# Optimization experiments

Hardware: AMD Instinct MI355X
Metric: run time of the kernel (lower is better)

## Reference

```python
import jax, jax.numpy as jnp
import numpy as np

D, K, N_NODES, E_DIM, H, L, HEADS, FF = 1024, 128, 200000, 384, 128, 2, 4, 128


def setup_inputs() -> dict:
    key = jax.random.key(0)
    ks = jax.random.split(key, 12)
    # regular graph: target node 0 has D neighbors (nodes 1..D); each neighbor n
    # has exactly K incoming edges, the first from tgt, the rest from random src != 0
    src = jax.random.randint(ks[0], (D, K), 1, N_NODES, dtype=jnp.int32)
    src = src.at[:, 0].set(0)
    dst = jnp.broadcast_to(jnp.arange(1, D + 1, dtype=jnp.int32)[:, None], (D, K))
    edge_index = jnp.stack([src.reshape(-1), dst.reshape(-1)])
    s = 0.05
    return {
        "tgt_x_index": jnp.zeros((1,), jnp.int32),
        "x": jax.random.normal(ks[1], (N_NODES, 64), jnp.float32),
        "edge_index": edge_index,
        "edge_attrs": jax.random.normal(ks[2], (D * K, E_DIM), jnp.float32),
        "first_token_marker": jax.random.normal(ks[3], (H,), jnp.float32),
        "proj_w": jax.random.normal(ks[4], (H, E_DIM), jnp.float32) * s,
        "proj_b": jnp.zeros((H,), jnp.float32),
        "attn_in_w": jax.random.normal(ks[5], (L, 3 * H, H), jnp.float32) * s,
        "attn_in_b": jnp.zeros((L, 3 * H), jnp.float32),
        "attn_out_w": jax.random.normal(ks[6], (L, H, H), jnp.float32) * s,
        "attn_out_b": jnp.zeros((L, H), jnp.float32),
        "ln1_g": jnp.ones((L, H), jnp.float32),
        "ln1_b": jnp.zeros((L, H), jnp.float32),
        "ff1_w": jax.random.normal(ks[7], (L, FF, H), jnp.float32) * s,
        "ff1_b": jnp.zeros((L, FF), jnp.float32),
        "ff2_w": jax.random.normal(ks[8], (L, H, FF), jnp.float32) * s,
        "ff2_b": jnp.zeros((L, H), jnp.float32),
        "ln2_g": jnp.ones((L, H), jnp.float32),
        "ln2_b": jnp.zeros((L, H), jnp.float32),
        "pred_w1": jax.random.normal(ks[9], (H, H), jnp.float32) * s,
        "pred_b1": jnp.zeros((H,), jnp.float32),
        "pred_w2": jax.random.normal(ks[10], (1, H), jnp.float32) * s,
        "pred_b2": jnp.zeros((1,), jnp.float32),
        "num_neighbors": D,
        "seq_len": K,
    }


def _ln(x, g, b):
    m = x.mean(-1, keepdims=True)
    v = ((x - m) ** 2).mean(-1, keepdims=True)
    return (x - m) * jax.lax.rsqrt(v + 1e-5) * g + b


def _forward(tgt_x_index, x, edge_index, edge_attrs, first_token_marker,
             proj_w, proj_b, attn_in_w, attn_in_b, attn_out_w, attn_out_b,
             ln1_g, ln1_b, ff1_w, ff1_b, ff2_w, ff2_b, ln2_g, ln2_b,
             pred_w1, pred_b1, pred_w2, pred_b2, num_neighbors, seq_len):
    tgt = tgt_x_index[0]
    src, dst = edge_index[0], edge_index[1]
    is_tgt = src == tgt
    # neighbors of target, in edge order (torch: edge_index[1][edge_index[0]==tgt])
    neigh_idx = jnp.nonzero(is_tgt, size=num_neighbors)[0]
    neigh_nodes = dst[neigh_idx]                       # [D]
    # fused ragged gather: map each edge to its neighbor slot, sort so that each
    # neighbor's edges are contiguous with the tgt->n edge first (stable sort
    # preserves original edge order within groups, matching boolean-mask gather)
    slot = jnp.full((x.shape[0],), num_neighbors, jnp.int32).at[neigh_nodes].set(
        jnp.arange(num_neighbors, dtype=jnp.int32))
    eslot = slot[dst]                                  # [E]
    sort_key = eslot.astype(jnp.int64) * 2 + jnp.where(is_tgt, 0, 1)
    order = jnp.argsort(sort_key)[: num_neighbors * seq_len]
    rows = edge_attrs[order].reshape(num_neighbors, seq_len, edge_attrs.shape[-1])
    hidden = proj_w.shape[0]
    hd = hidden // HEADS
    h = rows @ proj_w.T + proj_b                       # [D, K, H]
    h = h.at[:, 0, :].add(first_token_marker)          # first-token marker
    n_layers = attn_in_w.shape[0]
    for l in range(n_layers):
        qkv = h @ attn_in_w[l].T + attn_in_b[l]        # [D, K, 3H]
        q, k_, v = jnp.split(qkv, 3, axis=-1)
        q = q.reshape(num_neighbors, seq_len, HEADS, hd)
        k_ = k_.reshape(num_neighbors, seq_len, HEADS, hd)
        v = v.reshape(num_neighbors, seq_len, HEADS, hd)
        att = jax.nn.softmax(
            jnp.einsum('bqhd,bkhd->bhqk', q, k_) / jnp.sqrt(jnp.float32(hd)), axis=-1)
        o = jnp.einsum('bhqk,bkhd->bqhd', att, v).reshape(num_neighbors, seq_len, hidden)
        h = _ln(h + o @ attn_out_w[l].T + attn_out_b[l], ln1_g[l], ln1_b[l])
        f = jax.nn.relu(h @ ff1_w[l].T + ff1_b[l]) @ ff2_w[l].T + ff2_b[l]
        h = _ln(h + f, ln2_g[l], ln2_b[l])
    pooled = h.mean(axis=1)                            # mean over seq -> [D, H]
    final = pooled.mean(axis=0, keepdims=True)         # mean over neighbors -> [1, H]
    hmid = jax.nn.relu(final @ pred_w1.T + pred_b1)
    return jax.nn.sigmoid(hmid @ pred_w2.T + pred_b2)  # [1, 1]


def reference(tgt_x_index, x, edge_index, edge_attrs, first_token_marker,
              proj_w, proj_b, attn_in_w, attn_in_b, attn_out_w, attn_out_b,
              ln1_g, ln1_b, ff1_w, ff1_b, ff2_w, ff2_b, ln2_g, ln2_b,
              pred_w1, pred_b1, pred_w2, pred_b2, num_neighbors, seq_len):
    return _forward(tgt_x_index, x, edge_index, edge_attrs, first_token_marker,
                    proj_w, proj_b, attn_in_w, attn_in_b, attn_out_w, attn_out_b,
                    ln1_g, ln1_b, ff1_w, ff1_b, ff2_w, ff2_b, ln2_g, ln2_b,
                    pred_w1, pred_b1, pred_w2, pred_b2, num_neighbors, seq_len)
```

## Files before the change

### kernel.cpp

```cpp
#include <hip/hip_runtime.h>
#include <cstdint>
#include <cstddef>

#define D_N     1024
#define K_S     128
#define EDIM    384
#define HID     128
#define NHEAD   4
#define HDIM    32
#define FFD     128
#define NLAYER  2
#define ETOT    (D_N * K_S)
#define NNODES  200000
#define NBINS   (2 * D_N + 2)
#define NCH     512
#define CHL     (ETOT / NCH)

#define OFF_ORDER 0u
#define OFF_KEY   (1u << 19)
#define OFF_SLOT  (1u << 20)
#define OFF_HIST  (1u << 21)
#define OFF_TOT   (OFF_HIST + NBINS * NCH * 4)
#define OFF_POOL  (7u << 20)
#define OFF_WBF   OFF_HIST
#define WP_OFF 0
#define WI_OFF 49152
#define WO_OFF 147456
#define W1_OFF 180224
#define W2_OFF 212992
#define WTOT   245760

typedef __attribute__((ext_vector_type(8))) short  bf16x8;
typedef __attribute__((ext_vector_type(4))) short  short4v;
typedef __attribute__((ext_vector_type(4))) float  f32x4;

__device__ __forceinline__ short f2bf(float f) {
    union { float f; unsigned u; } v; v.f = f;
    unsigned r = v.u + 0x7fffu + ((v.u >> 16) & 1u);
    return (short)(r >> 16);
}
__device__ __forceinline__ int swz_off(int r, int byteInRow, int strideBytes) {
    return (r * strideBytes + byteInRow) ^ ((r & 7) << 4);
}

__global__ void init_ws(int* __restrict__ slot, int* __restrict__ hist)
{
    int idx = blockIdx.x * blockDim.x + threadIdx.x;
    int stride = gridDim.x * blockDim.x;
    for (int i = idx; i < NBINS * NCH; i += stride) hist[i] = 0;
    for (int i = idx; i < NNODES; i += stride) slot[i] = D_N;
}

__global__ void find_neigh(const int* __restrict__ eidx,
                           const int* __restrict__ tgt_idx,
                           int* __restrict__ slot)
{
    __shared__ int wtot[16];
    __shared__ int wbase_s[16];
    __shared__ int neigh[D_N];
    const int tid  = threadIdx.x;
    const int lane = tid & 63;
    const int wv   = tid >> 6;
    const int tgt  = tgt_idx[0];
    const int* src = eidx;
    const int* dst = eidx + ETOT;
    const int epc  = ETOT / 1024;
    const int e0   = tid * epc;

    int c = 0;
    const int4* s4 = (const int4*)(src + e0);
    #pragma unroll 8
    for (int i = 0; i < epc / 4; ++i) {
        int4 v = s4[i];
        c += (v.x == tgt) + (v.y == tgt) + (v.z == tgt) + (v.w == tgt);
    }
    int incl = c;
    #pragma unroll
    for (int d = 1; d < 64; d <<= 1) {
        int t = __shfl_up(incl, d, 64);
        if (lane >= d) incl += t;
    }
    if (lane == 63) wtot[wv] = incl;
    __syncthreads();
    if (tid < 16) {
        int s = 0;
        for (int j = 0; j < tid; ++j) s += wtot[j];
        wbase_s[tid] = s;
    }
    __syncthreads();
    int r = wbase_s[wv] + incl - c;
    for (int e = e0; e < e0 + epc; ++e) {
        if (src[e] == tgt) { if (r < D_N) neigh[r] = dst[e]; ++r; }
    }
    __syncthreads();
    int total = wbase_s[15] + wtot[15];
    if (tid < total && tid < D_N) slot[neigh[tid]] = tid;
}

__global__ void compute_key(const int* __restrict__ eidx,
                            const int* __restrict__ tgt_idx,
                            const int* __restrict__ slot,
                            int* __restrict__ key)
{
    int e = blockIdx.x * 256 + threadIdx.x;
    if (e >= ETOT) return;
    int tgt = tgt_idx[0];
    key[e] = slot[eidx[ETOT + e]] * 2 + ((eidx[e] != tgt) ? 1 : 0);
}

__global__ void hist_build(const int* __restrict__ key, int* __restrict__ hist)
{
    const int c = blockIdx.x * 256 + threadIdx.x;
    if (c >= NCH) return;
    const int4* kp = (const int4*)(key + c * CHL);
    int cur = -1, run = 0;
    for (int i = 0; i < CHL / 4; ++i) {
        int4 k4 = kp[i];
        #pragma unroll
        for (int j = 0; j < 4; ++j) {
            int k = (j == 0) ? k4.x : (j == 1) ? k4.y : (j == 2) ? k4.z : k4.w;
            if (k == cur) { ++run; }
            else {
                if (run) hist[cur * NCH + c] += run;
                cur = k; run = 1;
            }
        }
    }
    if (run) hist[cur * NCH + c] += run;
}

__global__ void scan_pass1(const int* __restrict__ hist, int* __restrict__ tot)
{
    int b = blockIdx.x * 256 + threadIdx.x;
    if (b >= NBINS) return;
    const int4* h = (const int4*)(hist + b * NCH);
    int s = 0;
    #pragma unroll 4
    for (int c = 0; c < NCH / 4; ++c) { int4 v = h[c]; s += v.x + v.y + v.z + v.w; }
    tot[b] = s;
}

#define SCN 2176
__global__ void scan_pass2(int* __restrict__ tot)
{
    __shared__ int A[SCN];
    __shared__ int B[SCN];
    const int tid = threadIdx.x;
    for (int i = tid; i < SCN; i += 1024) A[i] = (i < NBINS) ? tot[i] : 0;
    __syncthreads();
    int* cur = A; int* nxt = B;
    for (int s = 1; s < SCN; s <<= 1) {
        for (int i = tid; i < SCN; i += 1024) nxt[i] = (i >= s) ? cur[i] + cur[i - s] : cur[i];
        __syncthreads();
        int* t = cur; cur = nxt; nxt = t;
    }
    for (int i = tid; i < NBINS; i += 1024) tot[i] = (i == 0) ? 0 : cur[i - 1];
}

__global__ void scan_pass3(int* __restrict__ hist, const int* __restrict__ base)
{
    const int wvg  = (blockIdx.x * blockDim.x + threadIdx.x) >> 6;
    const int lane = threadIdx.x & 63;
    if (wvg >= NBINS) return;
    int* h = hist + wvg * NCH + lane * 8;
    int4 a = *(int4*)h;
    int4 b4 = *(int4*)(h + 4);
    int ls = a.x + a.y + a.z + a.w + b4.x + b4.y + b4.z + b4.w;
    int incl = ls;
    #pragma unroll
    for (int d = 1; d < 64; d <<= 1) {
        int t = __shfl_up(incl, d, 64);
        if (lane >= d) incl += t;
    }
    int run = base[wvg] + incl - ls;
    int4 o1, o2;
    o1.x = run; run += a.x;  o1.y = run; run += a.y;
    o1.z = run; run += a.z;  o1.w = run; run += a.w;
    o2.x = run; run += b4.x; o2.y = run; run += b4.y;
    o2.z = run; run += b4.z; o2.w = run; run += b4.w;
    *(int4*)h = o1;
    *(int4*)(h + 4) = o2;
}

__global__ void scatter_order(const int* __restrict__ key,
                              int* __restrict__ hist,
                              int* __restrict__ order)
{
    const int c = blockIdx.x * 256 + threadIdx.x;
    if (c >= NCH) return;
    const int e0 = c * CHL;
    const int4* kp = (const int4*)(key + e0);
    int cur = -1, pos = 0;
    for (int i = 0; i < CHL / 4; ++i) {
        int4 k4 = kp[i];
        #pragma unroll
        for (int j = 0; j < 4; ++j) {
            int k = (j == 0) ? k4.x : (j == 1) ? k4.y : (j == 2) ? k4.z : k4.w;
            if (k != cur) {
                if (cur >= 0) hist[cur * NCH + c] = pos;
                cur = k;
                pos = hist[k * NCH + c];
            }
            if (pos >= 0 && pos < ETOT) order[pos] = e0 + i * 4 + j;
            ++pos;
        }
    }
    if (cur >= 0) hist[cur * NCH + c] = pos;
}

__global__ void cvt_all(const float* __restrict__ p0, const float* __restrict__ p1,
                        const float* __restrict__ p2, const float* __restrict__ p3,
                        const float* __restrict__ p4, short* __restrict__ wbf)
{
    int i = (blockIdx.x * 256 + threadIdx.x) * 8;
    if (i >= WTOT) return;
    const float* s;
    if      (i < WI_OFF) s = p0 + i;
    else if (i < WO_OFF) s = p1 + (i - WI_OFF);
    else if (i < W1_OFF) s = p2 + (i - WO_OFF);
    else if (i < W2_OFF) s = p3 + (i - W1_OFF);
    else                 s = p4 + (i - W2_OFF);
    float4 a = *(const float4*)s;
    float4 b = *(const float4*)(s + 4);
    bf16x8 o;
    o[0] = f2bf(a.x); o[1] = f2bf(a.y); o[2] = f2bf(a.z); o[3] = f2bf(a.w);
    o[4] = f2bf(b.x); o[5] = f2bf(b.y); o[6] = f2bf(b.z); o[7] = f2bf(b.w);
    *(bf16x8*)(wbf + i) = o;
}

template<int CF, int KC, typename GetB>
__device__ __forceinline__ void gemm1(f32x4 (&acc)[CF],
    const char* aB, int aRow0, int aStride, int l15, int g, GetB getB)
{
    #pragma unroll
    for (int kc = 0; kc < KC; ++kc) {
        bf16x8 a = *(const bf16x8*)(aB + swz_off(aRow0 + l15, kc * 64 + g * 16, aStride));
        #pragma unroll
        for (int cf = 0; cf < CF; ++cf)
            acc[cf] = __builtin_amdgcn_mfma_f32_16x16x32_bf16(a, getB(cf, kc), acc[cf], 0, 0, 0);
    }
}

template<int ROWB>
__device__ __forceinline__ void stage_w(const char* __restrict__ gsrc, char* ldst,
                                        int nbytes, int tid)
{
    #pragma unroll 4
    for (int u = tid * 16; u < nbytes; u += 512 * 16) {
        int row = u / ROWB;
        int in  = u - row * ROWB;
        *(bf16x8*)(ldst + swz_off(row, in, ROWB)) = *(const bf16x8*)(gsrc + u);
    }
}

__device__ __forceinline__ void layer_norm1(f32x4 (&x)[8],
    const float* __restrict__ gg, const float* __restrict__ bb, int l15)
{
    float gv[8], bv[8];
    #pragma unroll
    for (int cf = 0; cf < 8; ++cf) { gv[cf] = gg[l15 + 16 * cf]; bv[cf] = bb[l15 + 16 * cf]; }
    #pragma unroll
    for (int rg = 0; rg < 4; ++rg) {
        float s = 0.f;
        #pragma unroll
        for (int cf = 0; cf < 8; ++cf) s += x[cf][rg];
        s += __shfl_xor(s, 1); s += __shfl_xor(s, 2);
        s += __shfl_xor(s, 4); s += __shfl_xor(s, 8);
        float mean = s * (1.f / 128.f);
        float v = 0.f;
        #pragma unroll
        for (int cf = 0; cf < 8; ++cf) { float d = x[cf][rg] - mean; v += d * d; }
        v += __shfl_xor(v, 1); v += __shfl_xor(v, 2);
        v += __shfl_xor(v, 4); v += __shfl_xor(v, 8);
        float rs = rsqrtf(v * (1.f / 128.f) + 1e-5f);
        #pragma unroll
        for (int cf = 0; cf < 8; ++cf)
            x[cf][rg] = (x[cf][rg] - mean) * rs * gv[cf] + bv[cf];
    }
}

#define LDS_TOTAL 163840
__global__ __launch_bounds__(512, 2) void fused_mfma(
    const float* __restrict__ edge_attrs,
    const float* __restrict__ ftm,
    const short* __restrict__ wP, const float* __restrict__ projb,
    const short* __restrict__ wI, const float* __restrict__ aib,
    const short* __restrict__ wO, const float* __restrict__ aob,
    const float* __restrict__ l1g, const float* __restrict__ l1b,
    const short* __restrict__ w1, const float* __restrict__ f1b,
    const short* __restrict__ w2, const float* __restrict__ f2b,
    const float* __restrict__ l2g, const float* __restrict__ l2b,
    const int*   __restrict__ order,
    float*       __restrict__ pooled)
{
    __shared__ __align__(16) char sm[LDS_TOTAL];
    char* hbf  = sm;
    char* wbuf = sm + 32768;
    char* act  = sm + 131072;
    char* k_l  = act;
    char* vT   = act + 8192;
    char* qOh  = act + 16384;
    char* Pch  = act + 24576;
    char* ebuf = act;
    char* ffb  = act;
    float* pool_s = (float*)act;

    const int tid  = threadIdx.x;
    const int w    = tid >> 6;
    const int l    = tid & 63;
    const int l15  = l & 15;
    const int g    = l >> 4;
    const int row0 = 16 * w;
    const int b    = blockIdx.x;

    f32x4 hx[8];

    {
        #pragma unroll
        for (int cf = 0; cf < 8; ++cf) {
            float bs = projb[l15 + 16 * cf];
            hx[cf] = (f32x4){bs, bs, bs, bs};
        }
        const int r_off = l >> 2;
        const int coff  = (l & 3) * 32;
        const int row   = row0 + r_off;
        const int rowIdx = order[b * K_S + row];
        const float* arow = edge_attrs + (size_t)rowIdx * EDIM;

        float4 v[8];
        #pragma unroll
        for (int j = 0; j < 8; ++j) v[j] = *(const float4*)(arow + coff + j * 4);

        stage_w<768>((const char*)wP, wbuf, 98304, tid);
        __syncthreads();

        #pragma unroll
        for (int ch = 0; ch < 3; ++ch) {
            #pragma unroll
            for (int j = 0; j < 4; ++j) {
                float4 a = v[2 * j], c = v[2 * j + 1];
                bf16x8 pk;
                pk[0] = f2bf(a.x); pk[1] = f2bf(a.y); pk[2] = f2bf(a.z); pk[3] = f2bf(a.w);
                pk[4] = f2bf(c.x); pk[5] = f2bf(c.y); pk[6] = f2bf(c.z); pk[7] = f2bf(c.w);
                *(bf16x8*)(ebuf + swz_off(row, coff * 2 + j * 16, 256)) = pk;
            }
            if (ch < 2) {
                #pragma unroll
                for (int j = 0; j < 8; ++j)
                    v[j] = *(const float4*)(arow + (ch + 1) * 128 + coff + j * 4);
            }
            gemm1<8, 4>(hx, ebuf, row0, 256, l15, g,
                [&](int cf, int kc) {
                    return *(const bf16x8*)(wbuf +
                        swz_off(l15 + 16 * cf, ch * 256 + kc * 64 + g * 16, 768));
                });
        }
        if (w == 0 && g == 0) {
            #pragma unroll
            for (int cf = 0; cf < 8; ++cf) hx[cf][0] += ftm[l15 + 16 * cf];
        }
        #pragma unroll
        for (int cf = 0; cf < 8; ++cf)
            #pragma unroll
            for (int rg = 0; rg < 4; ++rg)
                *(short*)(hbf + swz_off(row0 + g * 4 + rg, (l15 + 16 * cf) * 2, 256)) =
                    f2bf(hx[cf][rg]);
    }
    __syncthreads();

    for (int ly = 0; ly < NLAYER; ++ly) {
        const short* WIl = wI + (size_t)ly * 3 * HID * HID;
        const float* bI  = aib + ly * 3 * HID;
        const short* WOl = wO + (size_t)ly * HID * HID;
        const float* bO  = aob + ly * HID;
        const short* W1l = w1 + (size_t)ly * FFD * HID;
        const float* b1  = f1b + ly * FFD;
        const short* W2l = w2 + (size_t)ly * HID * FFD;
        const float* b2v = f2b + ly * HID;

        stage_w<256>((const char*)WIl, wbuf, 98304, tid);

        #pragma unroll
        for (int cf = 0; cf < 8; ++cf) {
            float bs = bO[l15 + 16 * cf];
            #pragma unroll
            for (int rg = 0; rg < 4; ++rg) hx[cf][rg] += bs;
        }
        __syncthreads();

        for (int hd = 0; hd < NHEAD; ++hd) {
            f32x4 acc[6];
            #pragma unroll
            for (int cf = 0; cf < 6; ++cf) {
                float bs = bI[(cf >> 1) * HID + hd * HDIM + l15 + 16 * (cf & 1)];
                acc[cf] = (f32x4){bs, bs, bs, bs};
            }
            gemm1<6, 4>(acc, hbf, row0, 256, l15, g,
                [&](int cf, int kc) {
                    int colw = (cf >> 1) * HID + hd * HDIM + l15 + 16 * (cf & 1);
                    return *(const bf16x8*)(wbuf + swz_off(colw, kc * 64 + g * 16, 256));
                });
            #pragma unroll
            for (int cf = 0; cf < 2; ++cf) {
                int dcol = (l15 + 16 * cf) * 2;
                #pragma unroll
                for (int rg = 0; rg < 4; ++rg) {
                    int row = row0 + g * 4 + rg;
                    *(short*)(qOh + swz_off(row, dcol, 64)) = f2bf(acc[cf][rg]);
                    *(short*)(k_l + swz_off(row, dcol, 64)) = f2bf(acc[2 + cf][rg]);
                }
                short4v pv;
                pv[0] = f2bf(acc[4 + cf][0]); pv[1] = f2bf(acc[4 + cf][1]);
                pv[2] = f2bf(acc[4 + cf][2]); pv[3] = f2bf(acc[4 + cf][3]);
                *(short4v*)(vT + swz_off(l15 + 16 * cf, (row0 + g * 4) * 2, 256)) = pv;
            }
            __syncthreads();

            f32x4 sc[8];
            #pragma unroll
            for (int cf = 0; cf < 8; ++cf) sc[cf] = (f32x4){0.f, 0.f, 0.f, 0.f};
            gemm1<8, 1>(sc, qOh, row0, 64, l15, g,
                [&](int cf, int kc) {
                    (void)kc;
                    return *(const bf16x8*)(k_l + swz_off(l15 + 16 * cf, g * 16, 64));
                });

            const float SC_ = 0.17677669529663687f;
            float inv_s[4];
            #pragma unroll
            for (int rg = 0; rg < 4; ++rg) {
                float mx = -1e30f;
                #pragma unroll
                for (int cf = 0; cf < 8; ++cf) {
                    sc[cf][rg] *= SC_;
                    mx = fmaxf(mx, sc[cf][rg]);
                }
                mx = fmaxf(mx, __shfl_xor(mx, 1)); mx = fmaxf(mx, __shfl_xor(mx, 2));
                mx = fmaxf(mx, __shfl_xor(mx, 4)); mx = fmaxf(mx, __shfl_xor(mx, 8));
                float sum = 0.f;
                #pragma unroll
                for (int cf = 0; cf < 8; ++cf) {
                    float e = __expf(sc[cf][rg] - mx);
                    sc[cf][rg] = e; sum += e;
                }
                sum += __shfl_xor(sum, 1); sum += __shfl_xor(sum, 2);
                sum += __shfl_xor(sum, 4); sum += __shfl_xor(sum, 8);
                inv_s[rg] = 1.f / sum;
            }

            f32x4 ov[2];
            ov[0] = (f32x4){0.f, 0.f, 0.f, 0.f};
            ov[1] = (f32x4){0.f, 0.f, 0.f, 0.f};
            #pragma unroll
            for (int cc = 0; cc < 4; ++cc) {
                #pragma unroll
                for (int q = 0; q < 2; ++q) {
                    int cfi = 2 * cc + q;
                    #pragma unroll
                    for (int rg = 0; rg < 4; ++rg)
                        *(short*)(Pch + swz_off(row0 + g * 4 + rg, (l15 + 16 * q) * 2, 64)) =
                            f2bf(sc[cfi][rg] * inv_s[rg]);
                }
                gemm1<2, 1>(ov, Pch, row0, 64, l15, g,
                    [&](int cf, int kc) {
                        (void)kc;
                        return *(const bf16x8*)(vT + swz_off(l15 + 16 * cf, cc * 64 + g * 16, 256));
                    });
            }
            #pragma unroll
            for (int cf = 0; cf < 2; ++cf)
                #pragma unroll
                for (int rg = 0; rg < 4; ++rg)
                    *(short*)(qOh + swz_off(row0 + g * 4 + rg, (l15 + 16 * cf) * 2, 64)) =
                        f2bf(ov[cf][rg]);
            gemm1<8, 1>(hx, qOh, row0, 64, l15, g,
                [&](int cf, int kc) {
                    (void)kc;
                    int col = l15 + 16 * cf;
                    return *(const bf16x8*)(WOl + (size_t)col * HID + hd * HDIM + g * 8);
                });
            __syncthreads();
        }

        stage_w<256>((const char*)W1l, wbuf,         32768, tid);
        stage_w<256>((const char*)W2l, wbuf + 32768, 32768, tid);

        layer_norm1(hx, l1g + ly * HID, l1b + ly * HID, l15);
        #pragma unroll
        for (int cf = 0; cf < 8; ++cf)
            #pragma unroll
            for (int rg = 0; rg < 4; ++rg)
                *(short*)(hbf + swz_off(row0 + g * 4 + rg, (l15 + 16 * cf) * 2, 256)) =
                    f2bf(hx[cf][rg]);
        __syncthreads();

        f32x4 ff[8];
        #pragma unroll
        for (int cf = 0; cf < 8; ++cf) {
            float bs = b1[l15 + 16 * cf];
            ff[cf] = (f32x4){bs, bs, bs, bs};
        }
        gemm1<8, 4>(ff, hbf, row0, 256, l15, g,
            [&](int cf, int kc) {
                return *(const bf16x8*)(wbuf + swz_off(l15 + 16 * cf, kc * 64 + g * 16, 256));
            });
        #pragma unroll
        for (int cf = 0; cf < 8; ++cf)
            #pragma unroll
            for (int rg = 0; rg < 4; ++rg)
                *(short*)(ffb + swz_off(row0 + g * 4 + rg, (l15 + 16 * cf) * 2, 256)) =
                    f2bf(fmaxf(ff[cf][rg], 0.f));

        f32x4 yy[8];
        #pragma unroll
        for (int cf = 0; cf < 8; ++cf) {
            float bs = b2v[l15 + 16 * cf];
            yy[cf] = (f32x4){bs, bs, bs, bs};
        }
        gemm1<8, 4>(yy, ffb, row0, 256, l15, g,
            [&](int cf, int kc) {
                return *(const bf16x8*)(wbuf + 32768 +
                    swz_off(l15 + 16 * cf, kc * 64 + g * 16, 256));
            });
        #pragma unroll
        for (int cf = 0; cf < 8; ++cf) yy[cf] += hx[cf];
        layer_norm1(yy, l2g + ly * HID, l2b + ly * HID, l15);
        #pragma unroll
        for (int cf = 0; cf < 8; ++cf) {
            hx[cf] = yy[cf];
            #pragma unroll
            for (int rg = 0; rg < 4; ++rg)
                *(short*)(hbf + swz_off(row0 + g * 4 + rg, (l15 + 16 * cf) * 2, 256)) =
                    f2bf(yy[cf][rg]);
        }
        __syncthreads();
    }

    #pragma unroll
    for (int cf = 0; cf < 8; ++cf) {
        float s = hx[cf][0] + hx[cf][1] + hx[cf][2] + hx[cf][3];
        s += __shfl_xor(s, 16); s += __shfl_xor(s, 32);
        if (g == 0) pool_s[w * 128 + l15 + 16 * cf] = s;
    }
    __syncthreads();
    if (tid < 128) {
        float s = 0.f;
        #pragma unroll
        for (int ww = 0; ww < 8; ++ww) s += pool_s[ww * 128 + tid];
        pooled[b * HID + tid] = s * (1.f / 128.f);
    }
}

__global__ void final_pred(const float* __restrict__ pooled,
                           const float* __restrict__ w1, const float* __restrict__ b1,
                           const float* __restrict__ w2, const float* __restrict__ b2,
                           float* __restrict__ out)
{
    __shared__ float part[4][HID];
    __shared__ float fin[HID];
    __shared__ float hm[HID];
    const int tid = threadIdx.x;
    const int f = tid & 127, q = tid >> 7;
    float s = 0.f;
    for (int bb = q * 256; bb < (q + 1) * 256; ++bb) s += pooled[bb * HID + f];
    part[q][f] = s;
    __syncthreads();
    if (tid < HID) {
        fin[tid] = (part[0][tid] + part[1][tid] + part[2][tid] + part[3][tid])
                   * (1.f / (float)D_N);
    }
    __syncthreads();
    if (tid < HID) {
        float a = b1[tid];
        for (int k = 0; k < HID; ++k) a += fin[k] * w1[tid * HID + k];
        hm[tid] = fmaxf(a, 0.f) * w2[tid];
    }
    __syncthreads();
    if (tid == 0) {
        float z = 0.f;
        for (int j = 0; j < HID; ++j) z += hm[j];
        z += b2[0];
        out[0] = 1.f / (1.f + __expf(-z));
    }
}

extern "C" void kernel_launch(void* const* d_in, const int* in_sizes, int n_in,
                              void* d_out, int out_size, void* d_ws, size_t ws_size,
                              hipStream_t stream)
{
    (void)in_sizes; (void)n_in; (void)out_size; (void)ws_size;

    const int*   tgt   = (const int*)  d_in[0];
    const int*   eidx  = (const int*)  d_in[2];
    const float* eattr = (const float*)d_in[3];
    const float* ftm   = (const float*)d_in[4];
    const float* projw = (const float*)d_in[5];
    const float* projb = (const float*)d_in[6];
    const float* aiw   = (const float*)d_in[7];
    const float* aib   = (const float*)d_in[8];
    const float* aow   = (const float*)d_in[9];
    const float* aob   = (const float*)d_in[10];
    const float* l1g   = (const float*)d_in[11];
    const float* l1b   = (const float*)d_in[12];
    const float* f1w   = (const float*)d_in[13];
    const float* f1b   = (const float*)d_in[14];
    const float* f2w   = (const float*)d_in[15];
    const float* f2b   = (const float*)d_in[16];
    const float* l2g   = (const float*)d_in[17];
    const float* l2b   = (const float*)d_in[18];
    const float* pw1   = (const float*)d_in[19];
    const float* pb1   = (const float*)d_in[20];
    const float* pw2   = (const float*)d_in[21];
    const float* pb2   = (const float*)d_in[22];

    char* ws = (char*)d_ws;
    int*   order  = (int*)  (ws + OFF_ORDER);
    int*   key    = (int*)  (ws + OFF_KEY);
    int*   slot   = (int*)  (ws + OFF_SLOT);
    int*   hist   = (int*)  (ws + OFF_HIST);
    int*   tot    = (int*)  (ws + OFF_TOT);
    float* pooled = (float*)(ws + OFF_POOL);
    short* wbf    = (short*)(ws + OFF_WBF);

    init_ws      <<<dim3(1024), dim3(256),  0, stream>>>(slot, hist);
    find_neigh   <<<dim3(1),    dim3(1024), 0, stream>>>(eidx, tgt, slot);
    compute_key  <<<dim3(512),  dim3(256),  0, stream>>>(eidx, tgt, slot, key);
    hist_build   <<<dim3(2),    dim3(256),  0, stream>>>(key, hist);
    scan_pass1   <<<dim3(9),    dim3(256),  0, stream>>>(hist, tot);
    scan_pass2   <<<dim3(1),    dim3(1024), 0, stream>>>(tot);
    scan_pass3   <<<dim3(513),  dim3(256),  0, stream>>>(hist, tot);
    scatter_order<<<dim3(2),    dim3(256),  0, stream>>>(key, hist, order);
    cvt_all      <<<dim3(120),  dim3(256),  0, stream>>>(projw, aiw, aow, f1w, f2w, wbf);

    fused_mfma<<<dim3(D_N), dim3(512), 0, stream>>>(
        eattr, ftm,
        wbf + WP_OFF, projb,
        wbf + WI_OFF, aib,
        wbf + WO_OFF, aob,
        l1g, l1b,
        wbf + W1_OFF, f1b,
        wbf + W2_OFF, f2b,
        l2g, l2b,
        order, pooled);

    final_pred<<<dim3(1), dim3(512), 0, stream>>>(pooled, pw1, pb1, pw2, pb2, (float*)d_out);
}
```

Before: 521.2 us.

## Read bf16 weights directly from global, shrink LDS, fuse init and convert kernels

Stops staging the projection, attention and FFN weights into LDS and has the MFMA B operands load straight from global/L2 memory. This cuts LDS from 160KB to 80KB, which lets more blocks fit per CU. Heads are now processed in pairs with one barrier per pair, and the weight conversion is merged into the workspace-init kernel, removing one launch. The risk is more global and L2 traffic with uncoalesced B-fragment loads in every GEMM. The workspace offsets are rearranged so the weight buffer no longer overlaps the histogram.

```diff
diff --git a/kernel.cpp b/kernel.cpp
--- a/kernel.cpp
+++ b/kernel.cpp
@@ -17,12 +17,12 @@
 #define CHL     (ETOT / NCH)
 
 #define OFF_ORDER 0u
-#define OFF_KEY   (1u << 19)
-#define OFF_SLOT  (1u << 20)
-#define OFF_HIST  (1u << 21)
-#define OFF_TOT   (OFF_HIST + NBINS * NCH * 4)
-#define OFF_POOL  (7u << 20)
-#define OFF_WBF   OFF_HIST
+#define OFF_KEY   0x080000u
+#define OFF_SLOT  0x100000u
+#define OFF_HIST  0x200000u
+#define OFF_TOT   0x601800u
+#define OFF_WBF   0x604000u
+#define OFF_POOL  0x680000u
 #define WP_OFF 0
 #define WI_OFF 49152
 #define WO_OFF 147456
@@ -43,12 +43,30 @@
     return (r * strideBytes + byteInRow) ^ ((r & 7) << 4);
 }
 
-__global__ void init_ws(int* __restrict__ slot, int* __restrict__ hist)
+__global__ void init_cvt(int* __restrict__ slot, int* __restrict__ hist,
+                         const float* __restrict__ p0, const float* __restrict__ p1,
+                         const float* __restrict__ p2, const float* __restrict__ p3,
+                         const float* __restrict__ p4, short* __restrict__ wbf)
 {
     int idx = blockIdx.x * blockDim.x + threadIdx.x;
     int stride = gridDim.x * blockDim.x;
     for (int i = idx; i < NBINS * NCH; i += stride) hist[i] = 0;
     for (int i = idx; i < NNODES; i += stride) slot[i] = D_N;
+    int i = idx * 8;
+    if (i < WTOT) {
+        const float* s;
+        if      (i < WI_OFF) s = p0 + i;
+        else if (i < WO_OFF) s = p1 + (i - WI_OFF);
+        else if (i < W1_OFF) s = p2 + (i - WO_OFF);
+        else if (i < W2_OFF) s = p3 + (i - W1_OFF);
+        else                 s = p4 + (i - W2_OFF);
+        float4 a = *(const float4*)s;
+        float4 b = *(const float4*)(s + 4);
+        bf16x8 o;
+        o[0] = f2bf(a.x); o[1] = f2bf(a.y); o[2] = f2bf(a.z); o[3] = f2bf(a.w);
+        o[4] = f2bf(b.x); o[5] = f2bf(b.y); o[6] = f2bf(b.z); o[7] = f2bf(b.w);
+        *(bf16x8*)(wbf + i) = o;
+    }
 }
 
 __global__ void find_neigh(const int* __restrict__ eidx,
@@ -208,48 +226,17 @@
     if (cur >= 0) hist[cur * NCH + c] = pos;
 }
 
-__global__ void cvt_all(const float* __restrict__ p0, const float* __restrict__ p1,
-                        const float* __restrict__ p2, const float* __restrict__ p3,
-                        const float* __restrict__ p4, short* __restrict__ wbf)
-{
-    int i = (blockIdx.x * 256 + threadIdx.x) * 8;
-    if (i >= WTOT) return;
-    const float* s;
-    if      (i < WI_OFF) s = p0 + i;
-    else if (i < WO_OFF) s = p1 + (i - WI_OFF);
-    else if (i < W1_OFF) s = p2 + (i - WO_OFF);
-    else if (i < W2_OFF) s = p3 + (i - W1_OFF);
-    else                 s = p4 + (i - W2_OFF);
-    float4 a = *(const float4*)s;
-    float4 b = *(const float4*)(s + 4);
-    bf16x8 o;
-    o[0] = f2bf(a.x); o[1] = f2bf(a.y); o[2] = f2bf(a.z); o[3] = f2bf(a.w);
-    o[4] = f2bf(b.x); o[5] = f2bf(b.y); o[6] = f2bf(b.z); o[7] = f2bf(b.w);
-    *(bf16x8*)(wbf + i) = o;
-}
-
 template<int CF, int KC, typename GetB>
 __device__ __forceinline__ void gemm1(f32x4 (&acc)[CF],
-    const char* aB, int aRow0, int aStride, int l15, int g, GetB getB)
+    const char* aB, int aRow0, int aStride, int aColOff, int l15, int g, GetB getB)
 {
     #pragma unroll
     for (int kc = 0; kc < KC; ++kc) {
-        bf16x8 a = *(const bf16x8*)(aB + swz_off(aRow0 + l15, kc * 64 + g * 16, aStride));
+        bf16x8 a = *(const bf16x8*)(aB +
+            swz_off(aRow0 + l15, aColOff + kc * 64 + g * 16, aStride));
         #pragma unroll
         for (int cf = 0; cf < CF; ++cf)
             acc[cf] = __builtin_amdgcn_mfma_f32_16x16x32_bf16(a, getB(cf, kc), acc[cf], 0, 0, 0);
-    }
-}
-
-template<int ROWB>
-__device__ __forceinline__ void stage_w(const char* __restrict__ gsrc, char* ldst,
-                                        int nbytes, int tid)
-{
-    #pragma unroll 4
-    for (int u = tid * 16; u < nbytes; u += 512 * 16) {
-        int row = u / ROWB;
-        int in  = u - row * ROWB;
-        *(bf16x8*)(ldst + swz_off(row, in, ROWB)) = *(const bf16x8*)(gsrc + u);
     }
 }
 
@@ -279,7 +266,7 @@
     }
 }
 
-#define LDS_TOTAL 163840
+#define LDS_TOTAL 81920
 __global__ __launch_bounds__(512, 2) void fused_mfma(
     const float* __restrict__ edge_attrs,
     const float* __restrict__ ftm,
@@ -294,16 +281,12 @@
     float*       __restrict__ pooled)
 {
     __shared__ __align__(16) char sm[LDS_TOTAL];
-    char* hbf  = sm;
-    char* wbuf = sm + 32768;
-    char* act  = sm + 131072;
-    char* k_l  = act;
-    char* vT   = act + 8192;
-    char* qOh  = act + 16384;
-    char* Pch  = act + 24576;
-    char* ebuf = act;
-    char* ffb  = act;
-    float* pool_s = (float*)act;
+    char* hbf = sm;
+    char* q01 = sm + 32768;
+    char* k01 = sm + 49152;
+    char* vT  = sm + 65536;
+    char* ebuf = sm + 32768;
+    float* pool_s = (float*)(sm + 32768);
 
     const int tid  = threadIdx.x;
     const int w    = tid >> 6;
@@ -330,9 +313,6 @@
         float4 v[8];
         #pragma unroll
         for (int j = 0; j < 8; ++j) v[j] = *(const float4*)(arow + coff + j * 4);
-
-        stage_w<768>((const char*)wP, wbuf, 98304, tid);
-        __syncthreads();
 
         #pragma unroll
         for (int ch = 0; ch < 3; ++ch) {
@@ -349,10 +329,10 @@
                 for (int j = 0; j < 8; ++j)
                     v[j] = *(const float4*)(arow + (ch + 1) * 128 + coff + j * 4);
             }
-            gemm1<8, 4>(hx, ebuf, row0, 256, l15, g,
+            gemm1<8, 4>(hx, ebuf, row0, 256, 0, l15, g,
                 [&](int cf, int kc) {
-                    return *(const bf16x8*)(wbuf +
-                        swz_off(l15 + 16 * cf, ch * 256 + kc * 64 + g * 16, 768));
+                    return *(const bf16x8*)(wP +
+                        (size_t)(l15 + 16 * cf) * EDIM + ch * 128 + kc * 32 + g * 8);
                 });
         }
         if (w == 0 && g == 0) {
@@ -378,112 +358,119 @@
         const short* W2l = w2 + (size_t)ly * HID * FFD;
         const float* b2v = f2b + ly * HID;
 
-        stage_w<256>((const char*)WIl, wbuf, 98304, tid);
-
         #pragma unroll
         for (int cf = 0; cf < 8; ++cf) {
             float bs = bO[l15 + 16 * cf];
             #pragma unroll
             for (int rg = 0; rg < 4; ++rg) hx[cf][rg] += bs;
         }
-        __syncthreads();
-
-        for (int hd = 0; hd < NHEAD; ++hd) {
-            f32x4 acc[6];
-            #pragma unroll
-            for (int cf = 0; cf < 6; ++cf) {
-                float bs = bI[(cf >> 1) * HID + hd * HDIM + l15 + 16 * (cf & 1)];
-                acc[cf] = (f32x4){bs, bs, bs, bs};
+
+        #pragma unroll
+        for (int hp = 0; hp < 2; ++hp) {
+            #pragma unroll
+            for (int hh = 0; hh < 2; ++hh) {
+                const int hd = hp * 2 + hh;
+                f32x4 acc[6];
+                #pragma unroll
+                for (int cf = 0; cf < 6; ++cf) {
+                    float bs = bI[(cf >> 1) * HID + hd * HDIM + l15 + 16 * (cf & 1)];
+                    acc[cf] = (f32x4){bs, bs, bs, bs};
+                }
+                gemm1<6, 4>(acc, hbf, row0, 256, 0, l15, g,
+                    [&](int cf, int kc) {
+                        int colw = (cf >> 1) * HID + hd * HDIM + l15 + 16 * (cf & 1);
+                        return *(const bf16x8*)(WIl + (size_t)colw * HID + kc * 32 + g * 8);
+                    });
+                #pragma unroll
+                for (int cf = 0; cf < 2; ++cf) {
+                    int dcol = hh * 64 + (l15 + 16 * cf) * 2;
+                    #pragma unroll
+                    for (int rg = 0; rg < 4; ++rg) {
+                        int row = row0 + g * 4 + rg;
+                        *(short*)(q01 + swz_off(row, dcol, 128)) = f2bf(acc[cf][rg]);
+                        *(short*)(k01 + swz_off(row, dcol, 128)) = f2bf(acc[2 + cf][rg]);
+                    }
+                    short4v pv;
+                    pv[0] = f2bf(acc[4 + cf][0]); pv[1] = f2bf(acc[4 + cf][1]);
+                    pv[2] = f2bf(acc[4 + cf][2]); pv[3] = f2bf(acc[4 + cf][3]);
+                    *(short4v*)(vT + swz_off(hh * 32 + l15 + 16 * cf,
+                                             (row0 + g * 4) * 2, 256)) = pv;
+                }
             }
-            gemm1<6, 4>(acc, hbf, row0, 256, l15, g,
-                [&](int cf, int kc) {
-                    int colw = (cf >> 1) * HID + hd * HDIM + l15 + 16 * (cf & 1);
-                    return *(const bf16x8*)(wbuf + swz_off(colw, kc * 64 + g * 16, 256));
-                });
-            #pragma unroll
-            for (int cf = 0; cf < 2; ++cf) {
-                int dcol = (l15 + 16 * cf) * 2;
+            __syncthreads();
+
+            #pragma unroll
+            for (int hh = 0; hh < 2; ++hh) {
+                const int hd = hp * 2 + hh;
+                f32x4 sc[8];
+                #pragma unroll
+                for (int cf = 0; cf < 8; ++cf) sc[cf] = (f32x4){0.f, 0.f, 0.f, 0.f};
+                gemm1<8, 1>(sc, q01, row0, 128, hh * 64, l15, g,
+                    [&](int cf, int kc) {
+                        (void)kc;
+                        return *(const bf16x8*)(k01 +
+                            swz_off(l15 + 16 * cf, hh * 64 + g * 16, 128));
+                    });
+
+                const float SC_ = 0.17677669529663687f;
+                float inv_s[4];
                 #pragma unroll
                 for (int rg = 0; rg < 4; ++rg) {
-                    int row = row0 + g * 4 + rg;
-                    *(short*)(qOh + swz_off(row, dcol, 64)) = f2bf(acc[cf][rg]);
-                    *(short*)(k_l + swz_off(row, dcol, 64)) = f2bf(acc[2 + cf][rg]);
+                    float mx = -1e30f;
+                    #pragma unroll
+                    for (int cf = 0; cf < 8; ++cf) {
+                        sc[cf][rg] *= SC_;
+                        mx = fmaxf(mx, sc[cf][rg]);
+                    }
+                    mx = fmaxf(mx, __shfl_xor(mx, 1)); mx = fmaxf(mx, __shfl_xor(mx, 2));
+                    mx = fmaxf(mx, __shfl_xor(mx, 4)); mx = fmaxf(mx, __shfl_xor(mx, 8));
+                    float sum = 0.f;
+                    #pragma unroll
+                    for (int cf = 0; cf < 8; ++cf) {
+                        float e = __expf(sc[cf][rg] - mx);
+                        sc[cf][rg] = e; sum += e;
+                    }
+                    sum += __shfl_xor(sum, 1); sum += __shfl_xor(sum, 2);
+                    sum += __shfl_xor(sum, 4); sum += __shfl_xor(sum, 8);
+                    inv_s[rg] = 1.f / sum;
                 }
-                short4v pv;
-                pv[0] = f2bf(acc[4 + cf][0]); pv[1] = f2bf(acc[4 + cf][1]);
-                pv[2] = f2bf(acc[4 + cf][2]); pv[3] = f2bf(acc[4 + cf][3]);
-                *(short4v*)(vT + swz_off(l15 + 16 * cf, (row0 + g * 4) * 2, 256)) = pv;
+
+                f32x4 ov[2];
+                ov[0] = (f32x4){0.f, 0.f, 0.f, 0.f};
+                ov[1] = (f32x4){0.f, 0.f, 0.f, 0.f};
+                #pragma unroll
+                for (int cc = 0; cc < 4; ++cc) {
+                    #pragma unroll
+                    for (int q = 0; q < 2; ++q) {
+                        int cfi = 2 * cc + q;
+                        #pragma unroll
+                        for (int rg = 0; rg < 4; ++rg)
+                            *(short*)(q01 + swz_off(row0 + g * 4 + rg,
+                                hh * 64 + (l15 + 16 * q) * 2, 128)) =
+                                f2bf(sc[cfi][rg] * inv_s[rg]);
+                    }
+                    gemm1<2, 1>(ov, q01, row0, 128, hh * 64, l15, g,
+                        [&](int cf, int kc) {
+                            (void)kc;
+                            return *(const bf16x8*)(vT + swz_off(hh * 32 + l15 + 16 * cf,
+                                                                 cc * 64 + g * 16, 256));
+                        });
+                }
+                #pragma unroll
+                for (int cf = 0; cf < 2; ++cf)
+                    #pragma unroll
+                    for (int rg = 0; rg < 4; ++rg)
+                        *(short*)(q01 + swz_off(row0 + g * 4 + rg,
+                            hh * 64 + (l15 + 16 * cf) * 2, 128)) = f2bf(ov[cf][rg]);
+                gemm1<8, 1>(hx, q01, row0, 128, hh * 64, l15, g,
+                    [&](int cf, int kc) {
+                        (void)kc;
+                        return *(const bf16x8*)(WOl +
+                            (size_t)(l15 + 16 * cf) * HID + hd * HDIM + g * 8);
+                    });
             }
             __syncthreads();
-
-            f32x4 sc[8];
-            #pragma unroll
-            for (int cf = 0; cf < 8; ++cf) sc[cf] = (f32x4){0.f, 0.f, 0.f, 0.f};
-            gemm1<8, 1>(sc, qOh, row0, 64, l15, g,
-                [&](int cf, int kc) {
-                    (void)kc;
-                    return *(const bf16x8*)(k_l + swz_off(l15 + 16 * cf, g * 16, 64));
-                });
-
-            const float SC_ = 0.17677669529663687f;
-            float inv_s[4];
-            #pragma unroll
-            for (int rg = 0; rg < 4; ++rg) {
-                float mx = -1e30f;
-                #pragma unroll
-                for (int cf = 0; cf < 8; ++cf) {
-                    sc[cf][rg] *= SC_;
-                    mx = fmaxf(mx, sc[cf][rg]);
-                }
-                mx = fmaxf(mx, __shfl_xor(mx, 1)); mx = fmaxf(mx, __shfl_xor(mx, 2));
-                mx = fmaxf(mx, __shfl_xor(mx, 4)); mx = fmaxf(mx, __shfl_xor(mx, 8));
-                float sum = 0.f;
-                #pragma unroll
-                for (int cf = 0; cf < 8; ++cf) {
-                    float e = __expf(sc[cf][rg] - mx);
-                    sc[cf][rg] = e; sum += e;
-                }
-                sum += __shfl_xor(sum, 1); sum += __shfl_xor(sum, 2);
-                sum += __shfl_xor(sum, 4); sum += __shfl_xor(sum, 8);
-                inv_s[rg] = 1.f / sum;
-            }
-
-            f32x4 ov[2];
-            ov[0] = (f32x4){0.f, 0.f, 0.f, 0.f};
-            ov[1] = (f32x4){0.f, 0.f, 0.f, 0.f};
-            #pragma unroll
-            for (int cc = 0; cc < 4; ++cc) {
-                #pragma unroll
-                for (int q = 0; q < 2; ++q) {
-                    int cfi = 2 * cc + q;
-                    #pragma unroll
-                    for (int rg = 0; rg < 4; ++rg)
-                        *(short*)(Pch + swz_off(row0 + g * 4 + rg, (l15 + 16 * q) * 2, 64)) =
-                            f2bf(sc[cfi][rg] * inv_s[rg]);
-                }
-                gemm1<2, 1>(ov, Pch, row0, 64, l15, g,
-                    [&](int cf, int kc) {
-                        (void)kc;
-                        return *(const bf16x8*)(vT + swz_off(l15 + 16 * cf, cc * 64 + g * 16, 256));
-                    });
-            }
-            #pragma unroll
-            for (int cf = 0; cf < 2; ++cf)
-                #pragma unroll
-                for (int rg = 0; rg < 4; ++rg)
-                    *(short*)(qOh + swz_off(row0 + g * 4 + rg, (l15 + 16 * cf) * 2, 64)) =
-                        f2bf(ov[cf][rg]);
-            gemm1<8, 1>(hx, qOh, row0, 64, l15, g,
-                [&](int cf, int kc) {
-                    (void)kc;
-                    int col = l15 + 16 * cf;
-                    return *(const bf16x8*)(WOl + (size_t)col * HID + hd * HDIM + g * 8);
-                });
-            __syncthreads();
-        }
-
-        stage_w<256>((const char*)W1l, wbuf,         32768, tid);
-        stage_w<256>((const char*)W2l, wbuf + 32768, 32768, tid);
+        }
 
         layer_norm1(hx, l1g + ly * HID, l1b + ly * HID, l15);
         #pragma unroll
@@ -492,7 +479,6 @@
             for (int rg = 0; rg < 4; ++rg)
                 *(short*)(hbf + swz_off(row0 + g * 4 + rg, (l15 + 16 * cf) * 2, 256)) =
                     f2bf(hx[cf][rg]);
-        __syncthreads();
 
         f32x4 ff[8];
         #pragma unroll
@@ -500,15 +486,16 @@
             float bs = b1[l15 + 16 * cf];
             ff[cf] = (f32x4){bs, bs, bs, bs};
         }
-        gemm1<8, 4>(ff, hbf, row0, 256, l15, g,
+        gemm1<8, 4>(ff, hbf, row0, 256, 0, l15, g,
             [&](int cf, int kc) {
-                return *(const bf16x8*)(wbuf + swz_off(l15 + 16 * cf, kc * 64 + g * 16, 256));
+                return *(const bf16x8*)(W1l +
+                    (size_t)(l15 + 16 * cf) * HID + kc * 32 + g * 8);
             });
         #pragma unroll
         for (int cf = 0; cf < 8; ++cf)
             #pragma unroll
             for (int rg = 0; rg < 4; ++rg)
-                *(short*)(ffb + swz_off(row0 + g * 4 + rg, (l15 + 16 * cf) * 2, 256)) =
+                *(short*)(ebuf + swz_off(row0 + g * 4 + rg, (l15 + 16 * cf) * 2, 256)) =
                     f2bf(fmaxf(ff[cf][rg], 0.f));
 
         f32x4 yy[8];
@@ -517,10 +504,10 @@
             float bs = b2v[l15 + 16 * cf];
             yy[cf] = (f32x4){bs, bs, bs, bs};
         }
-        gemm1<8, 4>(yy, ffb, row0, 256, l15, g,
+        gemm1<8, 4>(yy, ebuf, row0, 256, 0, l15, g,
             [&](int cf, int kc) {
-                return *(const bf16x8*)(wbuf + 32768 +
-                    swz_off(l15 + 16 * cf, kc * 64 + g * 16, 256));
+                return *(const bf16x8*)(W2l +
+                    (size_t)(l15 + 16 * cf) * FFD + kc * 32 + g * 8);
             });
         #pragma unroll
         for (int cf = 0; cf < 8; ++cf) yy[cf] += hx[cf];
@@ -622,7 +609,8 @@
     float* pooled = (float*)(ws + OFF_POOL);
     short* wbf    = (short*)(ws + OFF_WBF);
 
-    init_ws      <<<dim3(1024), dim3(256),  0, stream>>>(slot, hist);
+    init_cvt     <<<dim3(1024), dim3(256),  0, stream>>>(slot, hist,
+                                                         projw, aiw, aow, f1w, f2w, wbf);
     find_neigh   <<<dim3(1),    dim3(1024), 0, stream>>>(eidx, tgt, slot);
     compute_key  <<<dim3(512),  dim3(256),  0, stream>>>(eidx, tgt, slot, key);
     hist_build   <<<dim3(2),    dim3(256),  0, stream>>>(key, hist);
@@ -630,7 +618,6 @@
     scan_pass2   <<<dim3(1),    dim3(1024), 0, stream>>>(tot);
     scan_pass3   <<<dim3(513),  dim3(256),  0, stream>>>(hist, tot);
     scatter_order<<<dim3(2),    dim3(256),  0, stream>>>(key, hist, order);
-    cvt_all      <<<dim3(120),  dim3(256),  0, stream>>>(projw, aiw, aow, f1w, f2w, wbf);
 
     fused_mfma<<<dim3(D_N), dim3(512), 0, stream>>>(
         eattr, ftm,
```

After: 803.3 us. 54.1% more time.

## Replace chunked histogram counting sort with atomic bin counts and scatter

Applied to the files above, without the earlier changes.

Builds the edge ordering with per-edge atomic bin counts, a single-block scan and an atomic scatter. This replaces the chunked histogram build, three scan passes and the serial two-block scatter. It also merges workspace initialisation with the weight bf16 conversion and drops the large histogram clear. The within-bin order becomes nondeterministic, which relies on the downstream attention and mean-pool being order-insensitive.

```diff
diff --git a/kernel.cpp b/kernel.cpp
--- a/kernel.cpp
+++ b/kernel.cpp
@@ -13,16 +13,13 @@
 #define ETOT    (D_N * K_S)
 #define NNODES  200000
 #define NBINS   (2 * D_N + 2)
-#define NCH     512
-#define CHL     (ETOT / NCH)
 
 #define OFF_ORDER 0u
-#define OFF_KEY   (1u << 19)
-#define OFF_SLOT  (1u << 20)
-#define OFF_HIST  (1u << 21)
-#define OFF_TOT   (OFF_HIST + NBINS * NCH * 4)
-#define OFF_POOL  (7u << 20)
-#define OFF_WBF   OFF_HIST
+#define OFF_KEY   0x080000u
+#define OFF_SLOT  0x100000u
+#define OFF_CNT   0x200000u
+#define OFF_WBF   0x210000u
+#define OFF_POOL  0x290000u
 #define WP_OFF 0
 #define WI_OFF 49152
 #define WO_OFF 147456
@@ -43,12 +40,30 @@
     return (r * strideBytes + byteInRow) ^ ((r & 7) << 4);
 }
 
-__global__ void init_ws(int* __restrict__ slot, int* __restrict__ hist)
+__global__ void init_cvt(int* __restrict__ slot, int* __restrict__ cnt,
+                         const float* __restrict__ p0, const float* __restrict__ p1,
+                         const float* __restrict__ p2, const float* __restrict__ p3,
+                         const float* __restrict__ p4, short* __restrict__ wbf)
 {
     int idx = blockIdx.x * blockDim.x + threadIdx.x;
     int stride = gridDim.x * blockDim.x;
-    for (int i = idx; i < NBINS * NCH; i += stride) hist[i] = 0;
     for (int i = idx; i < NNODES; i += stride) slot[i] = D_N;
+    if (idx < NBINS) cnt[idx] = 0;
+    int i = idx * 8;
+    if (i < WTOT) {
+        const float* s;
+        if      (i < WI_OFF) s = p0 + i;
+        else if (i < WO_OFF) s = p1 + (i - WI_OFF);
+        else if (i < W1_OFF) s = p2 + (i - WO_OFF);
+        else if (i < W2_OFF) s = p3 + (i - W1_OFF);
+        else                 s = p4 + (i - W2_OFF);
+        float4 a = *(const float4*)s;
+        float4 b = *(const float4*)(s + 4);
+        bf16x8 o;
+        o[0] = f2bf(a.x); o[1] = f2bf(a.y); o[2] = f2bf(a.z); o[3] = f2bf(a.w);
+        o[4] = f2bf(b.x); o[5] = f2bf(b.y); o[6] = f2bf(b.z); o[7] = f2bf(b.w);
+        *(bf16x8*)(wbf + i) = o;
+    }
 }
 
 __global__ void find_neigh(const int* __restrict__ eidx,
@@ -97,56 +112,26 @@
     if (tid < total && tid < D_N) slot[neigh[tid]] = tid;
 }
 
-__global__ void compute_key(const int* __restrict__ eidx,
-                            const int* __restrict__ tgt_idx,
-                            const int* __restrict__ slot,
-                            int* __restrict__ key)
+__global__ void count_key(const int* __restrict__ eidx,
+                          const int* __restrict__ tgt_idx,
+                          const int* __restrict__ slot,
+                          int* __restrict__ key, int* __restrict__ cnt)
 {
     int e = blockIdx.x * 256 + threadIdx.x;
     if (e >= ETOT) return;
     int tgt = tgt_idx[0];
-    key[e] = slot[eidx[ETOT + e]] * 2 + ((eidx[e] != tgt) ? 1 : 0);
-}
-
-__global__ void hist_build(const int* __restrict__ key, int* __restrict__ hist)
-{
-    const int c = blockIdx.x * 256 + threadIdx.x;
-    if (c >= NCH) return;
-    const int4* kp = (const int4*)(key + c * CHL);
-    int cur = -1, run = 0;
-    for (int i = 0; i < CHL / 4; ++i) {
-        int4 k4 = kp[i];
-        #pragma unroll
-        for (int j = 0; j < 4; ++j) {
-            int k = (j == 0) ? k4.x : (j == 1) ? k4.y : (j == 2) ? k4.z : k4.w;
-            if (k == cur) { ++run; }
-            else {
-                if (run) hist[cur * NCH + c] += run;
-                cur = k; run = 1;
-            }
-        }
-    }
-    if (run) hist[cur * NCH + c] += run;
-}
-
-__global__ void scan_pass1(const int* __restrict__ hist, int* __restrict__ tot)
-{
-    int b = blockIdx.x * 256 + threadIdx.x;
-    if (b >= NBINS) return;
-    const int4* h = (const int4*)(hist + b * NCH);
-    int s = 0;
-    #pragma unroll 4
-    for (int c = 0; c < NCH / 4; ++c) { int4 v = h[c]; s += v.x + v.y + v.z + v.w; }
-    tot[b] = s;
+    int k = slot[eidx[ETOT + e]] * 2 + ((eidx[e] != tgt) ? 1 : 0);
+    key[e] = k;
+    atomicAdd(&cnt[k], 1);
 }
 
 #define SCN 2176
-__global__ void scan_pass2(int* __restrict__ tot)
+__global__ void scan_bins(int* __restrict__ cnt)
 {
     __shared__ int A[SCN];
     __shared__ int B[SCN];
     const int tid = threadIdx.x;
-    for (int i = tid; i < SCN; i += 1024) A[i] = (i < NBINS) ? tot[i] : 0;
+    for (int i = tid; i < SCN; i += 1024) A[i] = (i < NBINS) ? cnt[i] : 0;
     __syncthreads();
     int* cur = A; int* nxt = B;
     for (int s = 1; s < SCN; s <<= 1) {
@@ -154,78 +139,17 @@
         __syncthreads();
         int* t = cur; cur = nxt; nxt = t;
     }
-    for (int i = tid; i < NBINS; i += 1024) tot[i] = (i == 0) ? 0 : cur[i - 1];
-}
-
-__global__ void scan_pass3(int* __restrict__ hist, const int* __restrict__ base)
-{
-    const int wvg  = (blockIdx.x * blockDim.x + threadIdx.x) >> 6;
-    const int lane = threadIdx.x & 63;
-    if (wvg >= NBINS) return;
-    int* h = hist + wvg * NCH + lane * 8;
-    int4 a = *(int4*)h;
-    int4 b4 = *(int4*)(h + 4);
-    int ls = a.x + a.y + a.z + a.w + b4.x + b4.y + b4.z + b4.w;
-    int incl = ls;
-    #pragma unroll
-    for (int d = 1; d < 64; d <<= 1) {
-        int t = __shfl_up(incl, d, 64);
-        if (lane >= d) incl += t;
-    }
-    int run = base[wvg] + incl - ls;
-    int4 o1, o2;
-    o1.x = run; run += a.x;  o1.y = run; run += a.y;
-    o1.z = run; run += a.z;  o1.w = run; run += a.w;
-    o2.x = run; run += b4.x; o2.y = run; run += b4.y;
-    o2.z = run; run += b4.z; o2.w = run; run += b4.w;
-    *(int4*)h = o1;
-    *(int4*)(h + 4) = o2;
-}
-
-__global__ void scatter_order(const int* __restrict__ key,
-                              int* __restrict__ hist,
-                              int* __restrict__ order)
-{
-    const int c = blockIdx.x * 256 + threadIdx.x;
-    if (c >= NCH) return;
-    const int e0 = c * CHL;
-    const int4* kp = (const int4*)(key + e0);
-    int cur = -1, pos = 0;
-    for (int i = 0; i < CHL / 4; ++i) {
-        int4 k4 = kp[i];
-        #pragma unroll
-        for (int j = 0; j < 4; ++j) {
-            int k = (j == 0) ? k4.x : (j == 1) ? k4.y : (j == 2) ? k4.z : k4.w;
-            if (k != cur) {
-                if (cur >= 0) hist[cur * NCH + c] = pos;
-                cur = k;
-                pos = hist[k * NCH + c];
-            }
-            if (pos >= 0 && pos < ETOT) order[pos] = e0 + i * 4 + j;
-            ++pos;
-        }
-    }
-    if (cur >= 0) hist[cur * NCH + c] = pos;
-}
-
-__global__ void cvt_all(const float* __restrict__ p0, const float* __restrict__ p1,
-                        const float* __restrict__ p2, const float* __restrict__ p3,
-                        const float* __restrict__ p4, short* __restrict__ wbf)
-{
-    int i = (blockIdx.x * 256 + threadIdx.x) * 8;
-    if (i >= WTOT) return;
-    const float* s;
-    if      (i < WI_OFF) s = p0 + i;
-    else if (i < WO_OFF) s = p1 + (i - WI_OFF);
-    else if (i < W1_OFF) s = p2 + (i - WO_OFF);
-    else if (i < W2_OFF) s = p3 + (i - W1_OFF);
-    else                 s = p4 + (i - W2_OFF);
-    float4 a = *(const float4*)s;
-    float4 b = *(const float4*)(s + 4);
-    bf16x8 o;
-    o[0] = f2bf(a.x); o[1] = f2bf(a.y); o[2] = f2bf(a.z); o[3] = f2bf(a.w);
-    o[4] = f2bf(b.x); o[5] = f2bf(b.y); o[6] = f2bf(b.z); o[7] = f2bf(b.w);
-    *(bf16x8*)(wbf + i) = o;
+    for (int i = tid; i < NBINS; i += 1024) cnt[i] = (i == 0) ? 0 : cur[i - 1];
+}
+
+__global__ void scatter_at(const int* __restrict__ key,
+                           int* __restrict__ base,
+                           int* __restrict__ order)
+{
+    int e = blockIdx.x * 256 + threadIdx.x;
+    if (e >= ETOT) return;
+    int pos = atomicAdd(&base[key[e]], 1);
+    if (pos < ETOT) order[pos] = e;
 }
 
 template<int CF, int KC, typename GetB>
@@ -617,20 +541,16 @@
     int*   order  = (int*)  (ws + OFF_ORDER);
     int*   key    = (int*)  (ws + OFF_KEY);
     int*   slot   = (int*)  (ws + OFF_SLOT);
-    int*   hist   = (int*)  (ws + OFF_HIST);
-    int*   tot    = (int*)  (ws + OFF_TOT);
+    int*   cnt    = (int*)  (ws + OFF_CNT);
     float* pooled = (float*)(ws + OFF_POOL);
     short* wbf    = (short*)(ws + OFF_WBF);
 
-    init_ws      <<<dim3(1024), dim3(256),  0, stream>>>(slot, hist);
-    find_neigh   <<<dim3(1),    dim3(1024), 0, stream>>>(eidx, tgt, slot);
-    compute_key  <<<dim3(512),  dim3(256),  0, stream>>>(eidx, tgt, slot, key);
-    hist_build   <<<dim3(2),    dim3(256),  0, stream>>>(key, hist);
-    scan_pass1   <<<dim3(9),    dim3(256),  0, stream>>>(hist, tot);
-    scan_pass2   <<<dim3(1),    dim3(1024), 0, stream>>>(tot);
-    scan_pass3   <<<dim3(513),  dim3(256),  0, stream>>>(hist, tot);
-    scatter_order<<<dim3(2),    dim3(256),  0, stream>>>(key, hist, order);
-    cvt_all      <<<dim3(120),  dim3(256),  0, stream>>>(projw, aiw, aow, f1w, f2w, wbf);
+    init_cvt  <<<dim3(2048), dim3(256),  0, stream>>>(slot, cnt,
+                                                      projw, aiw, aow, f1w, f2w, wbf);
+    find_neigh<<<dim3(1),    dim3(1024), 0, stream>>>(eidx, tgt, slot);
+    count_key <<<dim3(512),  dim3(256),  0, stream>>>(eidx, tgt, slot, key, cnt);
+    scan_bins <<<dim3(1),    dim3(1024), 0, stream>>>(cnt);
+    scatter_at<<<dim3(512),  dim3(256),  0, stream>>>(key, cnt, order);
 
     fused_mfma<<<dim3(D_N), dim3(512), 0, stream>>>(
         eattr, ftm,
```

Result: faster. 481.2 us (-7.7%).
